# Optimization experiments

Measured on AMD Instinct MI355X. Metric: run time of the kernel, lower is better.

## Reference

```python
import jax, jax.numpy as jnp
import numpy as np

N = 512          # width of every layer (dims = [N]*4)
C = 16           # synaptic channels
NLAYERS = 4      # len(dims)
LT = NLAYERS - 1 # layer transitions
B = NLAYERS + N  # bias_vector_size = len(dims) + max(dims)
AGG_IN = N + B   # aggregator input width


def setup_inputs() -> dict:
    key = jax.random.key(0)
    ks = jax.random.split(key, 11)
    f32 = jnp.float32
    def rn(k, shape, scale):
        return (jax.random.normal(k, shape, f32) * scale)
    return {
        "x":      jax.random.normal(ks[0], (N,), f32),
        # Single_VECs: Linear(1, C) per (post q, pre p)
        "vec_W":  rn(ks[1], (LT, N, N, C), 1.0),
        "vec_b":  rn(ks[2], (LT, N, N, C), 0.5),
        # Single_Synapse: Linear(C,3) -> tanh -> Linear(3,1) -> tanh, per (q,p)
        "syn_W1": rn(ks[3], (LT, N, N, 3, C), 1.0 / np.sqrt(C)),
        "syn_b1": rn(ks[4], (LT, N, N, 3), 0.1),
        "syn_W2": rn(ks[5], (LT, N, N, 3), 1.0 / np.sqrt(3.0)),
        "syn_b2": rn(ks[6], (LT, N, N), 0.1),
        # Node_Aggregator: Linear(N + B, 3) -> tanh -> Linear(3,1), per q
        "agg_W1": rn(ks[7], (LT, N, 3, AGG_IN), 1.0 / np.sqrt(AGG_IN)),
        "agg_b1": rn(ks[8], (LT, N, 3), 0.1),
        "agg_W2": rn(ks[9], (LT, N, 3), 1.0 / np.sqrt(3.0)),
        "agg_b2": rn(ks[10], (LT, N), 0.1),
    }


def reference(x, vec_W, vec_b, syn_W1, syn_b1, syn_W2, syn_b2,
              agg_W1, agg_b1, agg_W2, agg_b2):
    # layer code for destination layer l+1 (one-hot over NLAYERS)
    layer_codes = jnp.eye(NLAYERS, dtype=x.dtype)[1:1 + LT]   # [LT, NLAYERS]
    node_eye = jnp.eye(N, dtype=x.dtype)                       # node one-hot codes

    def step(a, p):
        vW, vb, sW1, sb1, sW2, sb2, aW1, ab1, aW2, ab2, lcode = p
        # VECs: tanh(Linear(1->C)) per edge; a[p] is the scalar pre-activation
        filtered = jnp.tanh(a[None, :, None] * vW + vb)                 # [N_post, N_pre, C]
        # Single_Synapse per edge
        h1 = jnp.tanh(jnp.einsum('qpoc,qpc->qpo', sW1, filtered) + sb1) # [q, p, 3]
        s = jnp.tanh(jnp.einsum('qpo,qpo->qp', sW2, h1) + sb2)          # [q, p]
        # Node_Aggregator over cat(synapse_activations, bias_vector)
        agg_in = jnp.concatenate(
            [s, jnp.broadcast_to(lcode, (N, NLAYERS)), node_eye], axis=1)  # [q, N+B]
        h = jnp.tanh(jnp.einsum('qkp,qp->qk', aW1, agg_in) + ab1)       # [q, 3]
        a_next = jnp.einsum('qk,qk->q', aW2, h) + ab2                   # [q] (no tanh on fc2)
        return a_next, None

    a_final, _ = jax.lax.scan(
        step, x,
        (vec_W, vec_b, syn_W1, syn_b1, syn_W2, syn_b2,
         agg_W1, agg_b1, agg_W2, agg_b2, layer_codes))
    # original prepends each node: net_out = [node_{N-1}, ..., node_0], shape [N, 1]
    return a_final[::-1].reshape(-1, 1)
```

## Files before the change

### kernel.cpp

```cpp
#include <hip/hip_runtime.h>
#include <math.h>

#define N 512
#define C 16
#define AGG_IN 1028

typedef float v4f __attribute__((ext_vector_type(4)));

__device__ __forceinline__ float fast_tanh(float x) {
    float ax = fabsf(x);
    float t  = __expf(-2.0f * ax);
    float r  = __fdividef(1.0f - t, 1.0f + t);
    return copysignf(r, x);
}

__device__ __forceinline__ v4f ld4(const float* p) {
    return *(const v4f*)p;
}

__global__ __launch_bounds__(512, 4) void dan_layer_kernel(
    const float* __restrict__ a_in,
    float*       __restrict__ a_out,
    const float* __restrict__ vec_W,
    const float* __restrict__ vec_b,
    const float* __restrict__ syn_W1,
    const float* __restrict__ syn_b1,
    const float* __restrict__ syn_W2,
    const float* __restrict__ syn_b2,
    const float* __restrict__ agg_W1,
    const float* __restrict__ agg_b1,
    const float* __restrict__ agg_W2,
    const float* __restrict__ agg_b2,
    int l, int reverse_out)
{
    const int q = blockIdx.x;
    const int t = threadIdx.x;
    const int j = t & 3;
    const int e = t >> 2;

    __shared__ float red[3][8];
    __shared__ float hsh[3];

    const size_t qbase = ((size_t)(l * N + q)) * N;
    const int jc = (j < 3) ? j : 2;
    const float* aW1q = agg_W1 + ((size_t)(l * N + q)) * 3 * AGG_IN + (size_t)jc * AGG_IN;

    float pv = 0.f;

    {
    }
    size_t edge0 = qbase + e;
    v4f w  = ld4(vec_W  + edge0 * C  + j * 4);
    v4f b  = ld4(vec_b  + edge0 * C  + j * 4);
    v4f s0 = ld4(syn_W1 + edge0 * 48 + 0 * C + j * 4);
    v4f s1 = ld4(syn_W1 + edge0 * 48 + 1 * C + j * 4);
    v4f s2 = ld4(syn_W1 + edge0 * 48 + 2 * C + j * 4);
    float av  = a_in[e];
    float b1x = syn_b1[edge0 * 3 + 0];
    float b1y = syn_b1[edge0 * 3 + 1];
    float b1z = syn_b1[edge0 * 3 + 2];
    float w2x = syn_W2[edge0 * 3 + 0];
    float w2y = syn_W2[edge0 * 3 + 1];
    float w2z = syn_W2[edge0 * 3 + 2];
    float bb2 = syn_b2[edge0];
    float aw  = aW1q[e];

    #pragma unroll
    for (int pass = 0; pass < 4; ++pass) {
        const v4f   cw = w, cb = b, cs0 = s0, cs1 = s1, cs2 = s2;
        const float cav = av;
        const float cb1x = b1x, cb1y = b1y, cb1z = b1z;
        const float cw2x = w2x, cw2y = w2y, cw2z = w2z;
        const float cbb2 = bb2, caw = aw;

        if (pass < 3) {
            const int pn = (pass + 1) * 128 + e;
            const size_t en = qbase + pn;
            w  = ld4(vec_W  + en * C  + j * 4);
            b  = ld4(vec_b  + en * C  + j * 4);
            s0 = ld4(syn_W1 + en * 48 + 0 * C + j * 4);
            s1 = ld4(syn_W1 + en * 48 + 1 * C + j * 4);
            s2 = ld4(syn_W1 + en * 48 + 2 * C + j * 4);
            av  = a_in[pn];
            b1x = syn_b1[en * 3 + 0];
            b1y = syn_b1[en * 3 + 1];
            b1z = syn_b1[en * 3 + 2];
            w2x = syn_W2[en * 3 + 0];
            w2y = syn_W2[en * 3 + 1];
            w2z = syn_W2[en * 3 + 2];
            bb2 = syn_b2[en];
            aw  = aW1q[pn];
        }

        float f0 = fast_tanh(fmaf(cav, cw.x, cb.x));
        float f1 = fast_tanh(fmaf(cav, cw.y, cb.y));
        float f2 = fast_tanh(fmaf(cav, cw.z, cb.z));
        float f3 = fast_tanh(fmaf(cav, cw.w, cb.w));

        float d0 = fmaf(cs0.x, f0, fmaf(cs0.y, f1, fmaf(cs0.z, f2, cs0.w * f3)));
        float d1 = fmaf(cs1.x, f0, fmaf(cs1.y, f1, fmaf(cs1.z, f2, cs1.w * f3)));
        float d2 = fmaf(cs2.x, f0, fmaf(cs2.y, f1, fmaf(cs2.z, f2, cs2.w * f3)));

        d0 += __shfl_xor(d0, 1, 64);  d0 += __shfl_xor(d0, 2, 64);
        d1 += __shfl_xor(d1, 1, 64);  d1 += __shfl_xor(d1, 2, 64);
        d2 += __shfl_xor(d2, 1, 64);  d2 += __shfl_xor(d2, 2, 64);

        float h0 = fast_tanh(d0 + cb1x);
        float h1 = fast_tanh(d1 + cb1y);
        float h2 = fast_tanh(d2 + cb1z);
        float s = cbb2;
        s = fmaf(cw2x, h0, s);
        s = fmaf(cw2y, h1, s);
        s = fmaf(cw2z, h2, s);
        s = fast_tanh(s);

        if (j < 3) pv = fmaf(s, caw, pv);
    }

    pv += __shfl_xor(pv, 4, 64);
    pv += __shfl_xor(pv, 8, 64);
    pv += __shfl_xor(pv, 16, 64);
    pv += __shfl_xor(pv, 32, 64);

    const int wave = t >> 6;
    const int lane = t & 63;
    if (lane < 3) red[lane][wave] = pv;
    __syncthreads();

    if (t < 3) {
        const int k = t;
        float acc = 0.f;
        #pragma unroll
        for (int w8 = 0; w8 < 8; ++w8) acc += red[k][w8];
        const float* aW1 = agg_W1 + ((size_t)(l * N + q)) * 3 * AGG_IN + (size_t)k * AGG_IN;
        acc += aW1[N + (l + 1)];
        acc += aW1[N + 4 + q];
        acc += agg_b1[((size_t)(l * N + q)) * 3 + k];
        hsh[k] = fast_tanh(acc);
    }
    __syncthreads();

    if (t == 0) {
        const float* aW2 = agg_W2 + ((size_t)(l * N + q)) * 3;
        float out = agg_b2[l * N + q];
        out = fmaf(aW2[0], hsh[0], out);
        out = fmaf(aW2[1], hsh[1], out);
        out = fmaf(aW2[2], hsh[2], out);
        if (reverse_out) a_out[N - 1 - q] = out;
        else             a_out[q] = out;
    }
}

extern "C" void kernel_launch(void* const* d_in, const int* in_sizes, int n_in,
                              void* d_out, int out_size, void* d_ws, size_t ws_size,
                              hipStream_t stream) {
    const float* x      = (const float*)d_in[0];
    const float* vec_W  = (const float*)d_in[1];
    const float* vec_b  = (const float*)d_in[2];
    const float* syn_W1 = (const float*)d_in[3];
    const float* syn_b1 = (const float*)d_in[4];
    const float* syn_W2 = (const float*)d_in[5];
    const float* syn_b2 = (const float*)d_in[6];
    const float* agg_W1 = (const float*)d_in[7];
    const float* agg_b1 = (const float*)d_in[8];
    const float* agg_W2 = (const float*)d_in[9];
    const float* agg_b2 = (const float*)d_in[10];
    float* out = (float*)d_out;

    float* a0 = (float*)d_ws;
    float* a1 = a0 + N;

    dan_layer_kernel<<<N, 512, 0, stream>>>(x,  a0,  vec_W, vec_b, syn_W1, syn_b1,
                                            syn_W2, syn_b2, agg_W1, agg_b1, agg_W2, agg_b2,
                                            0, 0);
    dan_layer_kernel<<<N, 512, 0, stream>>>(a0, a1,  vec_W, vec_b, syn_W1, syn_b1,
                                            syn_W2, syn_b2, agg_W1, agg_b1, agg_W2, agg_b2,
                                            1, 0);
    dan_layer_kernel<<<N, 512, 0, stream>>>(a1, out, vec_W, vec_b, syn_W1, syn_b1,
                                            syn_W2, syn_b2, agg_W1, agg_b1, agg_W2, agg_b2,
                                            2, 1);
}
```

Baseline: 325.8 us.

## Fuse three layer launches into one persistent kernel with grid barriers

Replaces the three per-layer launches with a single kernel of 256 blocks, each handling two output nodes per layer. A software global barrier built on atomic counters and a generation flag separates the layers, and a small init kernel resets it. This removes launch gaps and per-layer tail effects, but serialises the two nodes inside each block and uses half as many blocks per layer. It also relies on all 256 blocks being co-resident, otherwise the barrier can deadlock and only escapes through a spin guard.

```diff
diff --git a/kernel.cpp b/kernel.cpp
--- a/kernel.cpp
+++ b/kernel.cpp
@@ -4,6 +4,7 @@
 #define N 512
 #define C 16
 #define AGG_IN 1028
+#define NBLK 256
 
 typedef float v4f __attribute__((ext_vector_type(4)));
 
@@ -18,9 +19,16 @@
     return *(const v4f*)p;
 }
 
-__global__ __launch_bounds__(512, 4) void dan_layer_kernel(
-    const float* __restrict__ a_in,
-    float*       __restrict__ a_out,
+__global__ void bar_init_kernel(unsigned int* bar) {
+    atomicExch(&bar[0], 0u);
+    atomicExch(&bar[1], 0u);
+    atomicExch(&bar[2], 0u);
+    atomicExch(&bar[3], 0u);
+}
+
+__global__ __launch_bounds__(512, 2) void dan_fused_kernel(
+    const float* __restrict__ x,
+    float*       __restrict__ outp,
     const float* __restrict__ vec_W,
     const float* __restrict__ vec_b,
     const float* __restrict__ syn_W1,
@@ -31,123 +39,155 @@
     const float* __restrict__ agg_b1,
     const float* __restrict__ agg_W2,
     const float* __restrict__ agg_b2,
-    int l, int reverse_out)
+    float* a0, float* a1,
+    unsigned int* bar)
 {
-    const int q = blockIdx.x;
+    const int bid = blockIdx.x;
     const int t = threadIdx.x;
     const int j = t & 3;
     const int e = t >> 2;
+    const int jc = (j < 3) ? j : 2;
 
     __shared__ float red[3][8];
     __shared__ float hsh[3];
 
-    const size_t qbase = ((size_t)(l * N + q)) * N;
-    const int jc = (j < 3) ? j : 2;
-    const float* aW1q = agg_W1 + ((size_t)(l * N + q)) * 3 * AGG_IN + (size_t)jc * AGG_IN;
-
-    float pv = 0.f;
-
-    {
-    }
-    size_t edge0 = qbase + e;
-    v4f w  = ld4(vec_W  + edge0 * C  + j * 4);
-    v4f b  = ld4(vec_b  + edge0 * C  + j * 4);
-    v4f s0 = ld4(syn_W1 + edge0 * 48 + 0 * C + j * 4);
-    v4f s1 = ld4(syn_W1 + edge0 * 48 + 1 * C + j * 4);
-    v4f s2 = ld4(syn_W1 + edge0 * 48 + 2 * C + j * 4);
-    float av  = a_in[e];
-    float b1x = syn_b1[edge0 * 3 + 0];
-    float b1y = syn_b1[edge0 * 3 + 1];
-    float b1z = syn_b1[edge0 * 3 + 2];
-    float w2x = syn_W2[edge0 * 3 + 0];
-    float w2y = syn_W2[edge0 * 3 + 1];
-    float w2z = syn_W2[edge0 * 3 + 2];
-    float bb2 = syn_b2[edge0];
-    float aw  = aW1q[e];
-
-    #pragma unroll
-    for (int pass = 0; pass < 4; ++pass) {
-        const v4f   cw = w, cb = b, cs0 = s0, cs1 = s1, cs2 = s2;
-        const float cav = av;
-        const float cb1x = b1x, cb1y = b1y, cb1z = b1z;
-        const float cw2x = w2x, cw2y = w2y, cw2z = w2z;
-        const float cbb2 = bb2, caw = aw;
-
-        if (pass < 3) {
-            const int pn = (pass + 1) * 128 + e;
-            const size_t en = qbase + pn;
-            w  = ld4(vec_W  + en * C  + j * 4);
-            b  = ld4(vec_b  + en * C  + j * 4);
-            s0 = ld4(syn_W1 + en * 48 + 0 * C + j * 4);
-            s1 = ld4(syn_W1 + en * 48 + 1 * C + j * 4);
-            s2 = ld4(syn_W1 + en * 48 + 2 * C + j * 4);
-            av  = a_in[pn];
-            b1x = syn_b1[en * 3 + 0];
-            b1y = syn_b1[en * 3 + 1];
-            b1z = syn_b1[en * 3 + 2];
-            w2x = syn_W2[en * 3 + 0];
-            w2y = syn_W2[en * 3 + 1];
-            w2z = syn_W2[en * 3 + 2];
-            bb2 = syn_b2[en];
-            aw  = aW1q[pn];
+    for (int l = 0; l < 3; ++l) {
+        const float* a_in = (l == 0) ? x : ((l == 1) ? a0 : a1);
+
+        for (int qi = 0; qi < 2; ++qi) {
+            const int q = bid * 2 + qi;
+            const size_t qbase = ((size_t)(l * N + q)) * N;
+            const float* aW1q = agg_W1 + ((size_t)(l * N + q)) * 3 * AGG_IN
+                                       + (size_t)jc * AGG_IN;
+
+            float pv = 0.f;
+
+            size_t edge0 = qbase + e;
+            v4f w  = ld4(vec_W  + edge0 * C  + j * 4);
+            v4f b  = ld4(vec_b  + edge0 * C  + j * 4);
+            v4f s0 = ld4(syn_W1 + edge0 * 48 + 0 * C + j * 4);
+            v4f s1 = ld4(syn_W1 + edge0 * 48 + 1 * C + j * 4);
+            v4f s2 = ld4(syn_W1 + edge0 * 48 + 2 * C + j * 4);
+            float av  = a_in[e];
+            float b1x = syn_b1[edge0 * 3 + 0];
+            float b1y = syn_b1[edge0 * 3 + 1];
+            float b1z = syn_b1[edge0 * 3 + 2];
+            float w2x = syn_W2[edge0 * 3 + 0];
+            float w2y = syn_W2[edge0 * 3 + 1];
+            float w2z = syn_W2[edge0 * 3 + 2];
+            float bb2 = syn_b2[edge0];
+            float aw  = aW1q[e];
+
+            #pragma unroll
+            for (int pass = 0; pass < 4; ++pass) {
+                const v4f   cw = w, cb = b, cs0 = s0, cs1 = s1, cs2 = s2;
+                const float cav = av;
+                const float cb1x = b1x, cb1y = b1y, cb1z = b1z;
+                const float cw2x = w2x, cw2y = w2y, cw2z = w2z;
+                const float cbb2 = bb2, caw = aw;
+
+                if (pass < 3) {
+                    const int pn = (pass + 1) * 128 + e;
+                    const size_t en = qbase + pn;
+                    w  = ld4(vec_W  + en * C  + j * 4);
+                    b  = ld4(vec_b  + en * C  + j * 4);
+                    s0 = ld4(syn_W1 + en * 48 + 0 * C + j * 4);
+                    s1 = ld4(syn_W1 + en * 48 + 1 * C + j * 4);
+                    s2 = ld4(syn_W1 + en * 48 + 2 * C + j * 4);
+                    av  = a_in[pn];
+                    b1x = syn_b1[en * 3 + 0];
+                    b1y = syn_b1[en * 3 + 1];
+                    b1z = syn_b1[en * 3 + 2];
+                    w2x = syn_W2[en * 3 + 0];
+                    w2y = syn_W2[en * 3 + 1];
+                    w2z = syn_W2[en * 3 + 2];
+                    bb2 = syn_b2[en];
+                    aw  = aW1q[pn];
+                }
+
+                float f0 = fast_tanh(fmaf(cav, cw.x, cb.x));
+                float f1 = fast_tanh(fmaf(cav, cw.y, cb.y));
+                float f2 = fast_tanh(fmaf(cav, cw.z, cb.z));
+                float f3 = fast_tanh(fmaf(cav, cw.w, cb.w));
+
+                float d0 = fmaf(cs0.x, f0, fmaf(cs0.y, f1, fmaf(cs0.z, f2, cs0.w * f3)));
+                float d1 = fmaf(cs1.x, f0, fmaf(cs1.y, f1, fmaf(cs1.z, f2, cs1.w * f3)));
+                float d2 = fmaf(cs2.x, f0, fmaf(cs2.y, f1, fmaf(cs2.z, f2, cs2.w * f3)));
+
+                d0 += __shfl_xor(d0, 1, 64);  d0 += __shfl_xor(d0, 2, 64);
+                d1 += __shfl_xor(d1, 1, 64);  d1 += __shfl_xor(d1, 2, 64);
+                d2 += __shfl_xor(d2, 1, 64);  d2 += __shfl_xor(d2, 2, 64);
+
+                float h0 = fast_tanh(d0 + cb1x);
+                float h1 = fast_tanh(d1 + cb1y);
+                float h2 = fast_tanh(d2 + cb1z);
+                float s = cbb2;
+                s = fmaf(cw2x, h0, s);
+                s = fmaf(cw2y, h1, s);
+                s = fmaf(cw2z, h2, s);
+                s = fast_tanh(s);
+
+                if (j < 3) pv = fmaf(s, caw, pv);
+            }
+
+            pv += __shfl_xor(pv, 4, 64);
+            pv += __shfl_xor(pv, 8, 64);
+            pv += __shfl_xor(pv, 16, 64);
+            pv += __shfl_xor(pv, 32, 64);
+
+            const int wave = t >> 6;
+            const int lane = t & 63;
+            __syncthreads();
+            if (lane < 3) red[lane][wave] = pv;
+            __syncthreads();
+
+            if (t < 3) {
+                const int k = t;
+                float acc = 0.f;
+                #pragma unroll
+                for (int w8 = 0; w8 < 8; ++w8) acc += red[k][w8];
+                const float* aW1 = agg_W1 + ((size_t)(l * N + q)) * 3 * AGG_IN
+                                          + (size_t)k * AGG_IN;
+                acc += aW1[N + (l + 1)];
+                acc += aW1[N + 4 + q];
+                acc += agg_b1[((size_t)(l * N + q)) * 3 + k];
+                hsh[k] = fast_tanh(acc);
+            }
+            __syncthreads();
+
+            if (t == 0) {
+                const float* aW2 = agg_W2 + ((size_t)(l * N + q)) * 3;
+                float o = agg_b2[l * N + q];
+                o = fmaf(aW2[0], hsh[0], o);
+                o = fmaf(aW2[1], hsh[1], o);
+                o = fmaf(aW2[2], hsh[2], o);
+                if (l == 0)      a0[q] = o;
+                else if (l == 1) a1[q] = o;
+                else             outp[N - 1 - q] = o;
+            }
         }
 
-        float f0 = fast_tanh(fmaf(cav, cw.x, cb.x));
-        float f1 = fast_tanh(fmaf(cav, cw.y, cb.y));
-        float f2 = fast_tanh(fmaf(cav, cw.z, cb.z));
-        float f3 = fast_tanh(fmaf(cav, cw.w, cb.w));
-
-        float d0 = fmaf(cs0.x, f0, fmaf(cs0.y, f1, fmaf(cs0.z, f2, cs0.w * f3)));
-        float d1 = fmaf(cs1.x, f0, fmaf(cs1.y, f1, fmaf(cs1.z, f2, cs1.w * f3)));
-        float d2 = fmaf(cs2.x, f0, fmaf(cs2.y, f1, fmaf(cs2.z, f2, cs2.w * f3)));
-
-        d0 += __shfl_xor(d0, 1, 64);  d0 += __shfl_xor(d0, 2, 64);
-        d1 += __shfl_xor(d1, 1, 64);  d1 += __shfl_xor(d1, 2, 64);
-        d2 += __shfl_xor(d2, 1, 64);  d2 += __shfl_xor(d2, 2, 64);
-
-        float h0 = fast_tanh(d0 + cb1x);
-        float h1 = fast_tanh(d1 + cb1y);
-        float h2 = fast_tanh(d2 + cb1z);
-        float s = cbb2;
-        s = fmaf(cw2x, h0, s);
-        s = fmaf(cw2y, h1, s);
-        s = fmaf(cw2z, h2, s);
-        s = fast_tanh(s);
-
-        if (j < 3) pv = fmaf(s, caw, pv);
-    }
-
-    pv += __shfl_xor(pv, 4, 64);
-    pv += __shfl_xor(pv, 8, 64);
-    pv += __shfl_xor(pv, 16, 64);
-    pv += __shfl_xor(pv, 32, 64);
-
-    const int wave = t >> 6;
-    const int lane = t & 63;
-    if (lane < 3) red[lane][wave] = pv;
-    __syncthreads();
-
-    if (t < 3) {
-        const int k = t;
-        float acc = 0.f;
-        #pragma unroll
-        for (int w8 = 0; w8 < 8; ++w8) acc += red[k][w8];
-        const float* aW1 = agg_W1 + ((size_t)(l * N + q)) * 3 * AGG_IN + (size_t)k * AGG_IN;
-        acc += aW1[N + (l + 1)];
-        acc += aW1[N + 4 + q];
-        acc += agg_b1[((size_t)(l * N + q)) * 3 + k];
-        hsh[k] = fast_tanh(acc);
-    }
-    __syncthreads();
-
-    if (t == 0) {
-        const float* aW2 = agg_W2 + ((size_t)(l * N + q)) * 3;
-        float out = agg_b2[l * N + q];
-        out = fmaf(aW2[0], hsh[0], out);
-        out = fmaf(aW2[1], hsh[1], out);
-        out = fmaf(aW2[2], hsh[2], out);
-        if (reverse_out) a_out[N - 1 - q] = out;
-        else             a_out[q] = out;
+        if (l < 2) {
+            __threadfence();
+            __syncthreads();
+            if (t == 0) {
+                unsigned int* cnt = bar + (size_t)l * 2;
+                unsigned int* gen = bar + (size_t)l * 2 + 1;
+                unsigned int g = atomicAdd(gen, 0u);
+                unsigned int v = atomicAdd(cnt, 1u);
+                if (v == NBLK - 1) {
+                    atomicExch(cnt, 0u);
+                    atomicAdd(gen, 1u);
+                } else {
+                    int guard = 0;
+                    while (atomicAdd(gen, 0u) == g) {
+                        __builtin_amdgcn_s_sleep(8);
+                        if (++guard > 4000000) break;
+                    }
+                }
+            }
+            __syncthreads();
+        }
     }
 }
 
@@ -169,14 +209,10 @@
 
     float* a0 = (float*)d_ws;
     float* a1 = a0 + N;
-
-    dan_layer_kernel<<<N, 512, 0, stream>>>(x,  a0,  vec_W, vec_b, syn_W1, syn_b1,
-                                            syn_W2, syn_b2, agg_W1, agg_b1, agg_W2, agg_b2,
-                                            0, 0);
-    dan_layer_kernel<<<N, 512, 0, stream>>>(a0, a1,  vec_W, vec_b, syn_W1, syn_b1,
-                                            syn_W2, syn_b2, agg_W1, agg_b1, agg_W2, agg_b2,
-                                            1, 0);
-    dan_layer_kernel<<<N, 512, 0, stream>>>(a1, out, vec_W, vec_b, syn_W1, syn_b1,
-                                            syn_W2, syn_b2, agg_W1, agg_b1, agg_W2, agg_b2,
-                                            2, 1);
-}
+    unsigned int* bar = (unsigned int*)(a0 + 2 * N);
+
+    bar_init_kernel<<<1, 1, 0, stream>>>(bar);
+    dan_fused_kernel<<<NBLK, 512, 0, stream>>>(
+        x, out, vec_W, vec_b, syn_W1, syn_b1, syn_W2, syn_b2,
+        agg_W1, agg_b1, agg_W2, agg_b2, a0, a1, bar);
+}
```

Result: slower. 418.9 us (+28.6%).
